# Performance work log

Measured on AMD Instinct MI355X. Metric: run time of the kernel, lower is better.

The kernel has to match this reference:

```python
import jax, jax.numpy as jnp
import numpy as np

INPUT_DIM = 362
HIDDEN = 256
STYLE_NUM = 60
OUTFIT_NUM = 49710
BATCH = 16384


def setup_inputs() -> dict:
    key = jax.random.key(0)
    ks = jax.random.split(key, 12)
    f32 = jnp.float32
    return {
        "i_feature": jax.random.normal(ks[0], (BATCH, INPUT_DIM), f32),
        "j_feature": jax.random.normal(ks[1], (BATCH, INPUT_DIM), f32),
        "k_feature": jax.random.normal(ks[2], (BATCH, INPUT_DIM), f32),
        # top_emb / bottom_emb Linear params (stored transposed: x @ W + b)
        "W_top": jax.random.normal(ks[3], (INPUT_DIM, HIDDEN), f32) * 0.05,
        "b_top": jnp.zeros((HIDDEN,), f32),
        "W_bot": jax.random.normal(ks[4], (INPUT_DIM, HIDDEN), f32) * 0.05,
        "b_bot": jnp.zeros((HIDDEN,), f32),
        # NMF factors (forward relu_'s them in place; we relu on use)
        "P_nmf": jax.random.normal(ks[5], (2 * INPUT_DIM, STYLE_NUM), f32),
        "N_nmf": jax.random.normal(ks[6], (2 * INPUT_DIM, STYLE_NUM), f32),
        "H1_nmf": jax.random.normal(ks[7], (STYLE_NUM, OUTFIT_NUM), f32),
        "H2_nmf": jax.random.normal(ks[8], (STYLE_NUM, OUTFIT_NUM), f32),
        "matirx_pos": jax.random.uniform(ks[9], (2 * INPUT_DIM, OUTFIT_NUM), f32),
        "matirx_neg": jax.random.uniform(ks[10], (2 * INPUT_DIM, OUTFIT_NUM), f32),
    }


def _emb(x, W, b):
    # nn.Sequential(Linear, Sigmoid)
    return jax.nn.sigmoid(x @ W + b)


def _style_score(i_f, j_f, styles, W_top, b_top, W_bot, b_bot):
    # Vectorized version of the per-sample loop:
    # squared-distance argmin codebook lookup + gather + rowwise dot.
    outfit = jnp.concatenate([i_f, j_f], axis=1)  # [B, 2D]
    # mean over feature dim of (x - s)^2; constant 1/(2D) scale does not change argmin
    d2 = (jnp.sum(outfit * outfit, axis=1, keepdims=True)
          - 2.0 * (outfit @ styles)
          + jnp.sum(styles * styles, axis=0, keepdims=True))  # [B, S]
    idx = jnp.argmin(d2, axis=1)                               # [B]
    sel = styles.T[idx]                                        # [B, 2D] gather
    top, bot = sel[:, :INPUT_DIM], sel[:, INPUT_DIM:]
    # diag(matmul) == rowwise dot
    return jnp.sum(_emb(top, W_top, b_top) * _emb(bot, W_bot, b_bot), axis=1)  # [B]


def reference(i_feature, j_feature, k_feature, W_top, b_top, W_bot, b_bot,
              P_nmf, N_nmf, H1_nmf, H2_nmf, matirx_pos, matirx_neg):
    Ti = _emb(i_feature, W_top, b_top)   # [B, H]
    Bj = _emb(j_feature, W_bot, b_bot)   # [B, H]
    Bk = _emb(k_feature, W_bot, b_bot)   # [B, H]
    # torch.diag(matmul(Ti, Bj.T)) == rowwise dot (avoids [B,B] intermediate)
    ij_score = jnp.sum(Ti * Bj, axis=1)  # [B]
    ik_score = jnp.sum(Ti * Bk, axis=1)  # [B]

    # forward does relu_ on .data before use
    P = jnp.maximum(P_nmf, 0.0)
    N = jnp.maximum(N_nmf, 0.0)
    H1 = jnp.maximum(H1_nmf, 0.0)
    H2 = jnp.maximum(H2_nmf, 0.0)

    style_ij = _style_score(i_feature, j_feature, P, W_top, b_top, W_bot, b_bot)
    style_ik = _style_score(i_feature, k_feature, N, W_top, b_top, W_bot, b_bot)

    # -mean(log(sigmoid(d))) computed stably
    loss1 = -jnp.mean(jax.nn.log_sigmoid(ij_score - ik_score))
    loss2 = -jnp.mean(jax.nn.log_sigmoid(style_ij - style_ik))
    loss3 = jnp.mean(jnp.square(matirx_pos - P @ H1)
                     + jnp.square(matirx_neg - N @ H2))
    loss = loss1 + loss2 + 0.1 * loss3

    ij_ik = jnp.stack([ij_score, ik_score], axis=1)  # [B, 2]
    auc = jnp.mean((jnp.argmax(ij_ik, axis=1) == 0).astype(jnp.float32))
    return (loss, loss1, loss2, loss3, auc)
```

## Files before the change

kernel.cpp:

```cpp
#include <hip/hip_runtime.h>
#include <math.h>

#define BATCH 16384
#define IND   362
#define KP    384
#define HID   256
#define STY   60
#define NOUT  49710
#define OUTP  51200
#define D2    724
#define D2P   768

#define NB_HR   3200
#define NB_CW   768
#define NB_CPN  384
#define NB_CF   9216
#define NB_CONV (NB_HR + NB_CW + NB_CPN + NB_CF)

#define NB_SS   120

#define N_DT    46
#define N_OC    25
#define OCHUNK  2048
#define NSTEP_CH 32
#define NB_M    (2 * N_DT * N_OC)

#define NB_EMB  1024
#define NB_SA   512
#define NB_HH   16
#define NB_PPB  2
#define NB_HEAD (NB_HH + NB_PPB)

typedef __bf16 bf16x8 __attribute__((ext_vector_type(8)));
typedef float  floatx4 __attribute__((ext_vector_type(4)));
typedef float  floatx2 __attribute__((ext_vector_type(2)));

__device__ inline floatx4 mfma16(bf16x8 a, bf16x8 b, floatx4 c) {
  return __builtin_amdgcn_mfma_f32_16x16x32_bf16(a, b, c, 0, 0, 0);
}

__device__ inline unsigned short f32_to_bf16(float x) {
  unsigned int u = __float_as_uint(x);
  unsigned int r = (u + 0x7FFFu + ((u >> 16) & 1u)) >> 16;
  return (unsigned short)r;
}

__device__ inline float sigm_fast(float x) { return 1.0f / (1.0f + __expf(-x)); }
__device__ inline float softplusf(float z) { return fmaxf(z, 0.0f) + log1pf(expf(-fabsf(z))); }

__global__ __launch_bounds__(256) void k_conv(
    const float* __restrict__ fi, const float* __restrict__ fj, const float* __restrict__ fk,
    const float* __restrict__ Wt, const float* __restrict__ Wb,
    const float* __restrict__ Pn, const float* __restrict__ Nn,
    const float* __restrict__ H1, const float* __restrict__ H2,
    unsigned short* __restrict__ fbf, unsigned short* __restrict__ wbfT,
    unsigned short* __restrict__ pnbfT, unsigned short* __restrict__ hrows) {
  int b = blockIdx.x;
  int t = threadIdx.x;

  if (b < NB_HR) {
    int e = (b * 256 + t) * 8;
    int row = e / OUTP;
    int o = e - row * OUTP;
    int s = row & 63;
    int mm = row >> 6;
    const float* H = mm ? H2 : H1;
    unsigned short* dst = hrows + (size_t)row * OUTP + o;
    unsigned int wv[4];
    if (s < STY && o + 8 <= NOUT) {
      const float* src = H + (size_t)s * NOUT + o;
      #pragma unroll
      for (int ee = 0; ee < 4; ee++) {
        floatx2 v = *(const floatx2*)(src + 2 * ee);
        wv[ee] = (unsigned)f32_to_bf16(fmaxf(v[0], 0.0f)) |
                 ((unsigned)f32_to_bf16(fmaxf(v[1], 0.0f)) << 16);
      }
    } else {
      #pragma unroll
      for (int ee = 0; ee < 4; ee++) {
        float lo = (s < STY && o + 2 * ee     < NOUT) ? fmaxf(H[(size_t)s * NOUT + o + 2 * ee],     0.0f) : 0.0f;
        float hi = (s < STY && o + 2 * ee + 1 < NOUT) ? fmaxf(H[(size_t)s * NOUT + o + 2 * ee + 1], 0.0f) : 0.0f;
        wv[ee] = (unsigned)f32_to_bf16(lo) | ((unsigned)f32_to_bf16(hi) << 16);
      }
    }
    uint4 v; v.x = wv[0]; v.y = wv[1]; v.z = wv[2]; v.w = wv[3];
    *(uint4*)dst = v;
    return;
  }
  b -= NB_HR;

  if (b < NB_CW) {
    int idx = b * 256 + t;
    int k = idx % KP;
    int rem = idx / KP;
    int h = rem % HID;
    int mm = rem / HID;
    const float* W = mm ? Wb : Wt;
    wbfT[idx] = f32_to_bf16(k < IND ? W[(size_t)k * HID + h] : 0.0f);
    return;
  }
  b -= NB_CW;

  if (b < NB_CPN) {
    int u = b * 256 + t;
    int s = u & 63;
    int v = u >> 6;
    int m = (v >= D2P) ? 1 : 0;
    int d = v - m * D2P;
    const float* M = m ? Nn : Pn;
    float x = (d < D2 && s < STY) ? fmaxf(M[(size_t)d * STY + s], 0.0f) : 0.0f;
    unsigned short bb = f32_to_bf16(x);
    int k = (d < IND) ? d : (d < D2 ? d + 22 : (d < 746 ? d - IND : d));
    pnbfT[((size_t)m * 64 + s) * D2P + k] = bb;
    return;
  }
  b -= NB_CPN;

  {
    long u = (long)b * 256 + t;
    int g = (int)(u % 48);
    long rf = u / 48;
    int row = (int)(rf % BATCH);
    int f = (int)(rf / BATCH);
    const float* src = (f == 0) ? fi : (f == 1 ? fj : fk);
    int d0 = g * 8;
    const float* sp = src + (size_t)row * IND + d0;
    unsigned int wv[4];
    #pragma unroll
    for (int e = 0; e < 4; e++) {
      int dd = d0 + 2 * e;
      float lo = (dd < IND)     ? sp[2 * e]     : 0.0f;
      float hi = (dd + 1 < IND) ? sp[2 * e + 1] : 0.0f;
      wv[e] = (unsigned)f32_to_bf16(lo) | ((unsigned)f32_to_bf16(hi) << 16);
    }
    uint4 v; v.x = wv[0]; v.y = wv[1]; v.z = wv[2]; v.w = wv[3];
    *(uint4*)(fbf + ((size_t)f * BATCH + row) * KP + d0) = v;
  }
}

__global__ __launch_bounds__(256) void k_style(
    const float* __restrict__ Wt, const float* __restrict__ btop,
    const float* __restrict__ Wb, const float* __restrict__ bbot,
    const float* __restrict__ Pn, const float* __restrict__ Nn,
    float* __restrict__ ss, float* __restrict__ cn) {
  __shared__ float sel[D2];
  __shared__ float shr[4];
  int b = blockIdx.x;
  int t = threadIdx.x;
  int s  = b % STY;
  int mt = b / STY;
  const float* M = mt ? Nn : Pn;
  float cnp = 0.0f;
  for (int d = t; d < D2; d += 256) {
    float v = fmaxf(M[(size_t)d * STY + s], 0.0f);
    sel[d] = v;
    cnp += v * v;
  }
  __syncthreads();
  float at = btop[t], ab = bbot[t];
  for (int d = 0; d < IND; d++) at = fmaf(sel[d],       Wt[(size_t)d * HID + t], at);
  for (int d = 0; d < IND; d++) ab = fmaf(sel[IND + d], Wb[(size_t)d * HID + t], ab);
  float prod = (1.0f / (1.0f + expf(-at))) * (1.0f / (1.0f + expf(-ab)));
  for (int off = 32; off > 0; off >>= 1) prod += __shfl_xor(prod, off);
  if ((t & 63) == 0) shr[t >> 6] = prod;
  __syncthreads();
  if (t == 0) ss[mt * 64 + s] = shr[0] + shr[1] + shr[2] + shr[3];
  __syncthreads();
  for (int off = 32; off > 0; off >>= 1) cnp += __shfl_xor(cnp, off);
  if ((t & 63) == 0) shr[t >> 6] = cnp;
  __syncthreads();
  if (t == 0) cn[mt * 64 + s] = shr[0] + shr[1] + shr[2] + shr[3];
}

__global__ __launch_bounds__(256, 4) void k_m(
    const unsigned short* __restrict__ hrows,
    const float* __restrict__ mp, const float* __restrict__ mneg,
    const float* __restrict__ Pn, const float* __restrict__ Nn,
    float* __restrict__ partial) {
  __shared__ float shp[4];
  int w = threadIdx.x >> 6, lane = threadIdx.x & 63;
  int m = lane & 15, q = lane >> 4;
  int b = blockIdx.x;
  int dt  = b % N_DT;
  int r   = b / N_DT;
  int oc  = r % N_OC;
  int mat = r / N_OC;
  int d0 = dt * 16, o0 = oc * OCHUNK;
  bool full = (o0 + OCHUNK <= NOUT);
  int d = d0 + m;
  bool rowok = (d < D2);
  const float* Mrow = (mat ? mneg : mp) + (size_t)d * NOUT;
  const unsigned short* Hb = hrows + ((size_t)mat * 64 + m) * OUTP;

  floatx4 acc[4];
  #pragma unroll
  for (int st = 0; st < 4; st++) acc[st] = (floatx4){0.f, 0.f, 0.f, 0.f};
  float msq = 0.0f;

  floatx2 mc[8], mn_[8];
  #pragma unroll
  for (int e = 0; e < 8; e++) { mc[e] = (floatx2){0.f, 0.f}; mn_[e] = (floatx2){0.f, 0.f}; }

  auto LOADM = [&](int j, floatx2* dst) {
    if (rowok) {
      if (full) {
        #pragma unroll
        for (int c = 0; c < 2; c++) {
          const float* Mr = Mrow + o0 + j * 64 + c * 32 + q * 8;
          dst[c * 4 + 0] = __builtin_nontemporal_load((const floatx2*)(Mr));
          dst[c * 4 + 1] = __builtin_nontemporal_load((const floatx2*)(Mr + 2));
          dst[c * 4 + 2] = __builtin_nontemporal_load((const floatx2*)(Mr + 4));
          dst[c * 4 + 3] = __builtin_nontemporal_load((const floatx2*)(Mr + 6));
        }
      } else {
        #pragma unroll
        for (int c = 0; c < 2; c++)
          #pragma unroll
          for (int e = 0; e < 4; e++) {
            int o = o0 + j * 64 + c * 32 + q * 8 + 2 * e;
            floatx2 v = {0.f, 0.f};
            if (o     < NOUT) v[0] = Mrow[o];
            if (o + 1 < NOUT) v[1] = Mrow[o + 1];
            dst[c * 4 + e] = v;
          }
      }
    } else {
      #pragma unroll
      for (int e = 0; e < 8; e++) dst[e] = (floatx2){0.f, 0.f};
    }
  };

  LOADM(w, mc);
  for (int j = w; j < NSTEP_CH; j += 4) {
    if (j + 4 < NSTEP_CH) LOADM(j + 4, mn_);
    bf16x8 h[2][4];
    #pragma unroll
    for (int c = 0; c < 2; c++)
      #pragma unroll
      for (int st = 0; st < 4; st++)
        h[c][st] = *(const bf16x8*)(Hb + (size_t)(st * 16) * OUTP + o0 + j * 64 + c * 32 + q * 8);
    #pragma unroll
    for (int c = 0; c < 2; c++) {
      union { unsigned int u32[4]; bf16x8 v; } cv;
      #pragma unroll
      for (int e = 0; e < 4; e++) {
        floatx2 tv = mc[c * 4 + e];
        msq = fmaf(tv[0], tv[0], msq);
        msq = fmaf(tv[1], tv[1], msq);
        cv.u32[e] = (unsigned)f32_to_bf16(tv[0]) | ((unsigned)f32_to_bf16(tv[1]) << 16);
      }
      #pragma unroll
      for (int st = 0; st < 4; st++) acc[st] = mfma16(cv.v, h[c][st], acc[st]);
    }
    #pragma unroll
    for (int e = 0; e < 8; e++) mc[e] = mn_[e];
  }

  const float* PM = mat ? Nn : Pn;
  float t2 = 0.0f;
  #pragma unroll
  for (int st = 0; st < 4; st++) {
    int s = st * 16 + m;
    if (s < STY) {
      #pragma unroll
      for (int rg = 0; rg < 4; rg++) {
        int dd = d0 + q * 4 + rg;
        if (dd < D2) {
          float pv = fmaxf(PM[(size_t)dd * STY + s], 0.0f);
          t2 = fmaf(pv, acc[st][rg], t2);
        }
      }
    }
  }
  float local = msq - 2.0f * t2;
  for (int off = 32; off > 0; off >>= 1) local += __shfl_xor(local, off);
  if (lane == 0) shp[w] = local;
  __syncthreads();
  if (threadIdx.x == 0) partial[blockIdx.x] = shp[0] + shp[1] + shp[2] + shp[3];
}

__global__ __launch_bounds__(256, 4) void k_emb(
    const unsigned short* __restrict__ fbf, const unsigned short* __restrict__ wbfT,
    const float* __restrict__ btop, const float* __restrict__ bbot,
    float* __restrict__ sIJ, float* __restrict__ sIK) {
  int w = threadIdx.x >> 6, lane = threadIdx.x & 63;
  int m = lane & 15, q = lane >> 4;
  int b = blockIdx.x;
  int r0 = (b & 255) * 64 + w * 16;
  int hb = (b >> 8) * 64;
  const unsigned short* fi = fbf + (size_t)(r0 + m) * KP + q * 8;
  const unsigned short* fj = fi + (size_t)BATCH * KP;
  const unsigned short* fk = fj + (size_t)BATCH * KP;
  floatx4 accI[4], accJ[4], accK[4];
  #pragma unroll
  for (int nt = 0; nt < 4; nt++) {
    accI[nt] = (floatx4){0.f, 0.f, 0.f, 0.f};
    accJ[nt] = (floatx4){0.f, 0.f, 0.f, 0.f};
    accK[nt] = (floatx4){0.f, 0.f, 0.f, 0.f};
  }
  for (int kc = 0; kc < 12; kc++) {
    bf16x8 ai = *(const bf16x8*)(fi + kc * 32);
    bf16x8 aj = *(const bf16x8*)(fj + kc * 32);
    bf16x8 ak = *(const bf16x8*)(fk + kc * 32);
    #pragma unroll
    for (int nt = 0; nt < 4; nt++) {
      int n = hb + nt * 16 + m;
      const unsigned short* wp = wbfT + (size_t)n * KP + kc * 32 + q * 8;
      bf16x8 bt8 = *(const bf16x8*)(wp);
      bf16x8 bb8 = *(const bf16x8*)(wp + (size_t)HID * KP);
      accI[nt] = mfma16(ai, bt8, accI[nt]);
      accJ[nt] = mfma16(aj, bb8, accJ[nt]);
      accK[nt] = mfma16(ak, bb8, accK[nt]);
    }
  }
  float sij[4] = {0.f, 0.f, 0.f, 0.f}, sik[4] = {0.f, 0.f, 0.f, 0.f};
  #pragma unroll
  for (int nt = 0; nt < 4; nt++) {
    int n = hb + nt * 16 + m;
    float vbt = btop[n], vbb = bbot[n];
    #pragma unroll
    for (int reg = 0; reg < 4; reg++) {
      float ti = sigm_fast(accI[nt][reg] + vbt);
      float tj = sigm_fast(accJ[nt][reg] + vbb);
      float tk = sigm_fast(accK[nt][reg] + vbb);
      sij[reg] += ti * tj;
      sik[reg] += ti * tk;
    }
  }
  #pragma unroll
  for (int reg = 0; reg < 4; reg++) {
    for (int off = 1; off < 16; off <<= 1) {
      sij[reg] += __shfl_xor(sij[reg], off);
      sik[reg] += __shfl_xor(sik[reg], off);
    }
  }
  if (m == 0) {
    #pragma unroll
    for (int reg = 0; reg < 4; reg++) {
      int row = r0 + q * 4 + reg;
      atomicAdd(&sIJ[row], sij[reg]);
      atomicAdd(&sIK[row], sik[reg]);
    }
  }
}

__global__ __launch_bounds__(256, 4) void k_sa(
    const unsigned short* __restrict__ fbf, const unsigned short* __restrict__ pnbfT,
    const float* __restrict__ cn, const float* __restrict__ ss,
    float* __restrict__ stIJ, float* __restrict__ stIK) {
  int w = threadIdx.x >> 6, lane = threadIdx.x & 63;
  int m = lane & 15, q = lane >> 4;
  int b = blockIdx.x;
  int mat = w & 1;
  int r0 = b * 32 + (w >> 1) * 16;
  const unsigned short* fA = fbf + (size_t)(r0 + m) * KP + q * 8;
  const unsigned short* fB = fA + (size_t)(1 + mat) * BATCH * KP;
  const unsigned short* Bp = pnbfT + (size_t)mat * 64 * D2P + q * 8;
  floatx4 acc[4];
  #pragma unroll
  for (int nt = 0; nt < 4; nt++) acc[nt] = (floatx4){0.f, 0.f, 0.f, 0.f};
  for (int kc = 0; kc < 24; kc++) {
    bf16x8 a = (kc < 12) ? *(const bf16x8*)(fA + kc * 32)
                         : *(const bf16x8*)(fB + (kc - 12) * 32);
    #pragma unroll
    for (int nt = 0; nt < 4; nt++) {
      bf16x8 bb = *(const bf16x8*)(Bp + (size_t)(nt * 16 + m) * D2P + kc * 32);
      acc[nt] = mfma16(a, bb, acc[nt]);
    }
  }
  const float* cnm = cn + mat * 64;
  float bv[4]; int bi[4];
  #pragma unroll
  for (int reg = 0; reg < 4; reg++) { bv[reg] = __builtin_inff(); bi[reg] = 1 << 30; }
  #pragma unroll
  for (int nt = 0; nt < 4; nt++) {
    int s = nt * 16 + m;
    float c = cnm[s & 63];
    #pragma unroll
    for (int reg = 0; reg < 4; reg++) {
      float d2 = (s < STY) ? (c - 2.0f * acc[nt][reg]) : __builtin_inff();
      if (d2 < bv[reg] || (d2 == bv[reg] && s < bi[reg])) { bv[reg] = d2; bi[reg] = s; }
    }
  }
  for (int off = 1; off < 16; off <<= 1) {
    #pragma unroll
    for (int reg = 0; reg < 4; reg++) {
      float ov = __shfl_xor(bv[reg], off);
      int   oi = __shfl_xor(bi[reg], off);
      if (ov < bv[reg] || (ov == bv[reg] && oi < bi[reg])) { bv[reg] = ov; bi[reg] = oi; }
    }
  }
  if (m == 0) {
    float* dst = mat ? stIK : stIJ;
    const float* ssm = ss + mat * 64;
    #pragma unroll
    for (int reg = 0; reg < 4; reg++) dst[r0 + q * 4 + reg] = ssm[bi[reg]];
  }
}

__global__ __launch_bounds__(256) void k_head(
    const unsigned short* __restrict__ pnbfT, const unsigned short* __restrict__ hrows,
    float* __restrict__ HHb, float* __restrict__ PPb) {
  __shared__ float red[4096];
  int w = threadIdx.x >> 6, lane = threadIdx.x & 63;
  int m = lane & 15, q = lane >> 4;
  int b = blockIdx.x;
  bool isPP = (b >= NB_HH);
  int mat, chunk, nsteps, stride;
  const unsigned short* Rb;
  if (!isPP) { mat = b >> 3; chunk = b & 7; Rb = hrows + (size_t)mat * 64 * OUTP; stride = OUTP; nsteps = 200; }
  else       { mat = b - NB_HH; chunk = 0; Rb = pnbfT + (size_t)mat * 64 * D2P;  stride = D2P;  nsteps = 24;  }
  const unsigned short* Rm = Rb + (size_t)m * stride;

  floatx4 acc[4][4];
  #pragma unroll
  for (int a2 = 0; a2 < 4; a2++)
    #pragma unroll
    for (int b2 = 0; b2 < 4; b2++) acc[a2][b2] = (floatx4){0.f, 0.f, 0.f, 0.f};

  bf16x8 hc[4], hn[4];
  auto LD = [&](int j, bf16x8* h) {
    int k = (chunk * nsteps + j) * 32 + q * 8;
    #pragma unroll
    for (int st = 0; st < 4; st++)
      h[st] = *(const bf16x8*)(Rm + (size_t)(st * 16) * stride + k);
  };
  int j = w;
  LD(j, hc);
  for (; j < nsteps; j += 4) {
    if (j + 4 < nsteps) LD(j + 4, hn);
    #pragma unroll
    for (int a2 = 0; a2 < 4; a2++)
      #pragma unroll
      for (int b2 = 0; b2 < 4; b2++)
        acc[a2][b2] = mfma16(hc[a2], hc[b2], acc[a2][b2]);
    #pragma unroll
    for (int st = 0; st < 4; st++) hc[st] = hn[st];
  }
  for (int idx = threadIdx.x; idx < 4096; idx += 256) red[idx] = 0.f;
  __syncthreads();
  #pragma unroll
  for (int a2 = 0; a2 < 4; a2++)
    #pragma unroll
    for (int b2 = 0; b2 < 4; b2++)
      #pragma unroll
      for (int r = 0; r < 4; r++)
        atomicAdd(&red[(a2 * 16 + q * 4 + r) * 64 + b2 * 16 + m], acc[a2][b2][r]);
  __syncthreads();
  float* dst = (isPP ? PPb : HHb) + (size_t)mat * 4096;
  for (int idx = threadIdx.x; idx < 4096; idx += 256) atomicAdd(&dst[idx], red[idx]);
}

__global__ __launch_bounds__(256) void k_final(
    const float* __restrict__ sIJ, const float* __restrict__ sIK,
    const float* __restrict__ stIJ, const float* __restrict__ stIK,
    const float* __restrict__ l3partial,
    const float* __restrict__ HHb, const float* __restrict__ PPb,
    float* __restrict__ out) {
  int t = threadIdx.x;
  float l1 = 0.f, l2 = 0.f, ac = 0.f;
  for (int r = t; r < BATCH; r += 256) {
    float dij = sIJ[r] - sIK[r];
    l1 += softplusf(-dij);
    if (dij >= 0.0f) ac += 1.0f;
    float dst = stIJ[r] - stIK[r];
    l2 += softplusf(-dst);
  }
  double l3 = 0.0;
  for (int p = t; p < NB_M; p += 256) l3 += (double)l3partial[p];
  for (int idx = t; idx < 8192; idx += 256) l3 += (double)HHb[idx] * (double)PPb[idx];
  __shared__ float sh1[4], sh2[4], sh3[4];
  __shared__ double sh4[4];
  for (int off = 32; off > 0; off >>= 1) {
    l1 += __shfl_xor(l1, off);
    l2 += __shfl_xor(l2, off);
    ac += __shfl_xor(ac, off);
    l3 += __shfl_xor(l3, off);
  }
  if ((t & 63) == 0) { sh1[t >> 6] = l1; sh2[t >> 6] = l2; sh3[t >> 6] = ac; sh4[t >> 6] = l3; }
  __syncthreads();
  if (t == 0) {
    double L1 = 0, L2 = 0, AC = 0, L3 = 0;
    for (int i = 0; i < 4; i++) { L1 += sh1[i]; L2 += sh2[i]; AC += sh3[i]; L3 += sh4[i]; }
    L1 /= BATCH; L2 /= BATCH; AC /= BATCH;
    L3 /= ((double)D2 * (double)NOUT);
    out[0] = (float)(L1 + L2 + 0.1 * L3);
    out[1] = (float)L1;
    out[2] = (float)L2;
    out[3] = (float)L3;
    out[4] = (float)AC;
  }
}

extern "C" void kernel_launch(void* const* d_in, const int* in_sizes, int n_in,
                              void* d_out, int out_size, void* d_ws, size_t ws_size,
                              hipStream_t stream) {
  (void)in_sizes; (void)n_in; (void)out_size; (void)ws_size;
  const float* i_f  = (const float*)d_in[0];
  const float* j_f  = (const float*)d_in[1];
  const float* k_f  = (const float*)d_in[2];
  const float* W_t  = (const float*)d_in[3];
  const float* b_t  = (const float*)d_in[4];
  const float* W_b  = (const float*)d_in[5];
  const float* b_b  = (const float*)d_in[6];
  const float* P_n  = (const float*)d_in[7];
  const float* N_n  = (const float*)d_in[8];
  const float* H1   = (const float*)d_in[9];
  const float* H2   = (const float*)d_in[10];
  const float* Mp   = (const float*)d_in[11];
  const float* Mn   = (const float*)d_in[12];
  float* out = (float*)d_out;
  char* ws = (char*)d_ws;

  const size_t OFF_FBF   = 0;
  const size_t OFF_WBFT  = OFF_FBF   + (size_t)3 * BATCH * KP * 2;
  const size_t OFF_PNBFT = OFF_WBFT  + (size_t)2 * HID * KP * 2;
  const size_t OFF_HROWS = OFF_PNBFT + (size_t)2 * 64 * D2P * 2;
  const size_t OFF_SIJ   = OFF_HROWS + (size_t)2 * 64 * OUTP * 2;
  const size_t OFF_SIK   = OFF_SIJ   + (size_t)BATCH * 4;
  const size_t OFF_HH    = OFF_SIK   + (size_t)BATCH * 4;
  const size_t OFF_PP    = OFF_HH    + (size_t)2 * 4096 * 4;
  const size_t OFF_STIJ  = OFF_PP    + (size_t)2 * 4096 * 4;
  const size_t OFF_STIK  = OFF_STIJ  + (size_t)BATCH * 4;
  const size_t OFF_SS    = OFF_STIK  + (size_t)BATCH * 4;
  const size_t OFF_CN    = OFF_SS    + 512;
  const size_t OFF_L3P   = OFF_CN    + 512;

  unsigned short* fbf   = (unsigned short*)(ws + OFF_FBF);
  unsigned short* wbfT  = (unsigned short*)(ws + OFF_WBFT);
  unsigned short* pnbfT = (unsigned short*)(ws + OFF_PNBFT);
  unsigned short* hrows = (unsigned short*)(ws + OFF_HROWS);
  float*  sIJ  = (float*)(ws + OFF_SIJ);
  float*  sIK  = (float*)(ws + OFF_SIK);
  float*  HHb  = (float*)(ws + OFF_HH);
  float*  PPb  = (float*)(ws + OFF_PP);
  float*  stIJ = (float*)(ws + OFF_STIJ);
  float*  stIK = (float*)(ws + OFF_STIK);
  float*  ss   = (float*)(ws + OFF_SS);
  float*  cn   = (float*)(ws + OFF_CN);
  float*  l3p  = (float*)(ws + OFF_L3P);

  hipMemsetAsync(ws + OFF_SIJ, 0, (size_t)BATCH * 4 * 2 + (size_t)4 * 4096 * 4, stream);

  k_conv<<<NB_CONV, 256, 0, stream>>>(i_f, j_f, k_f, W_t, W_b, P_n, N_n, H1, H2,
                                      fbf, wbfT, pnbfT, hrows);
  k_style<<<NB_SS, 256, 0, stream>>>(W_t, b_t, W_b, b_b, P_n, N_n, ss, cn);
  k_m<<<NB_M, 256, 0, stream>>>(hrows, Mp, Mn, P_n, N_n, l3p);
  k_emb<<<NB_EMB, 256, 0, stream>>>(fbf, wbfT, b_t, b_b, sIJ, sIK);
  k_sa<<<NB_SA, 256, 0, stream>>>(fbf, pnbfT, cn, ss, stIJ, stIK);
  k_head<<<NB_HEAD, 256, 0, stream>>>(pnbfT, hrows, HHb, PPb);
  k_final<<<1, 256, 0, stream>>>(sIJ, sIK, stIJ, stIK, l3p, HHb, PPb, out);
}
```

Measured before the change: 746.7 us.

## Restructure loss3 kernel to stage H chunk in LDS and sweep rows

The k_m kernel is reorganized so each block loads a 64x256 bf16 slice of H into swizzled shared memory once, then sweeps half of the 724 rows of the M matrix through it. Previously every block reloaded H from global for each 16-row tile. Relu'd P/N factors are now precomputed as a padded float layout in k_conv, so the epilogue reads them as vector loads instead of strided scalar loads. The H row padding is also reduced from 51200 to 49920 columns, which shrinks the conversion and head passes. The grid shrinks to 780 blocks and each thread holds 32 floatx2 of M in registers, which risks lower occupancy and less latency hiding on the dominant M stream.

```diff
diff --git a/kernel.cpp b/kernel.cpp
--- a/kernel.cpp
+++ b/kernel.cpp
@@ -7,11 +7,11 @@
 #define HID   256
 #define STY   60
 #define NOUT  49710
-#define OUTP  51200
+#define OUTP  49920
 #define D2    724
 #define D2P   768
 
-#define NB_HR   3200
+#define NB_HR   3120
 #define NB_CW   768
 #define NB_CPN  384
 #define NB_CF   9216
@@ -19,11 +19,11 @@
 
 #define NB_SS   120
 
-#define N_DT    46
-#define N_OC    25
-#define OCHUNK  2048
-#define NSTEP_CH 32
-#define NB_M    (2 * N_DT * N_OC)
+#define OCH     256
+#define N_OC    195
+#define DHALF   368
+#define NTILES  23
+#define NB_M    (2 * 2 * N_OC)
 
 #define NB_EMB  1024
 #define NB_SA   512
@@ -54,7 +54,8 @@
     const float* __restrict__ Pn, const float* __restrict__ Nn,
     const float* __restrict__ H1, const float* __restrict__ H2,
     unsigned short* __restrict__ fbf, unsigned short* __restrict__ wbfT,
-    unsigned short* __restrict__ pnbfT, unsigned short* __restrict__ hrows) {
+    unsigned short* __restrict__ pnbfT, unsigned short* __restrict__ hrows,
+    float* __restrict__ Pr) {
   int b = blockIdx.x;
   int t = threadIdx.x;
 
@@ -112,6 +113,7 @@
     unsigned short bb = f32_to_bf16(x);
     int k = (d < IND) ? d : (d < D2 ? d + 22 : (d < 746 ? d - IND : d));
     pnbfT[((size_t)m * 64 + s) * D2P + k] = bb;
+    Pr[((size_t)m * D2P + d) * 64 + s] = x;
     return;
   }
   b -= NB_CPN;
@@ -172,111 +174,118 @@
   if (t == 0) cn[mt * 64 + s] = shr[0] + shr[1] + shr[2] + shr[3];
 }
 
-__global__ __launch_bounds__(256, 4) void k_m(
-    const unsigned short* __restrict__ hrows,
+__global__ __launch_bounds__(256) void k_m(
+    const unsigned short* __restrict__ hrows, const float* __restrict__ Pr,
     const float* __restrict__ mp, const float* __restrict__ mneg,
-    const float* __restrict__ Pn, const float* __restrict__ Nn,
     float* __restrict__ partial) {
-  __shared__ float shp[4];
+  __shared__ unsigned short Hs[64 * OCH];
+  __shared__ float red[4];
   int w = threadIdx.x >> 6, lane = threadIdx.x & 63;
   int m = lane & 15, q = lane >> 4;
+
   int b = blockIdx.x;
-  int dt  = b % N_DT;
-  int r   = b / N_DT;
-  int oc  = r % N_OC;
-  int mat = r / N_OC;
-  int d0 = dt * 16, o0 = oc * OCHUNK;
-  bool full = (o0 + OCHUNK <= NOUT);
-  int d = d0 + m;
-  bool rowok = (d < D2);
-  const float* Mrow = (mat ? mneg : mp) + (size_t)d * NOUT;
-  const unsigned short* Hb = hrows + ((size_t)mat * 64 + m) * OUTP;
-
-  floatx4 acc[4];
-  #pragma unroll
-  for (int st = 0; st < 4; st++) acc[st] = (floatx4){0.f, 0.f, 0.f, 0.f};
-  float msq = 0.0f;
-
-  floatx2 mc[8], mn_[8];
-  #pragma unroll
-  for (int e = 0; e < 8; e++) { mc[e] = (floatx2){0.f, 0.f}; mn_[e] = (floatx2){0.f, 0.f}; }
-
-  auto LOADM = [&](int j, floatx2* dst) {
-    if (rowok) {
-      if (full) {
-        #pragma unroll
-        for (int c = 0; c < 2; c++) {
-          const float* Mr = Mrow + o0 + j * 64 + c * 32 + q * 8;
-          dst[c * 4 + 0] = __builtin_nontemporal_load((const floatx2*)(Mr));
-          dst[c * 4 + 1] = __builtin_nontemporal_load((const floatx2*)(Mr + 2));
-          dst[c * 4 + 2] = __builtin_nontemporal_load((const floatx2*)(Mr + 4));
-          dst[c * 4 + 3] = __builtin_nontemporal_load((const floatx2*)(Mr + 6));
-        }
-      } else {
-        #pragma unroll
-        for (int c = 0; c < 2; c++)
-          #pragma unroll
-          for (int e = 0; e < 4; e++) {
-            int o = o0 + j * 64 + c * 32 + q * 8 + 2 * e;
-            floatx2 v = {0.f, 0.f};
-            if (o     < NOUT) v[0] = Mrow[o];
-            if (o + 1 < NOUT) v[1] = Mrow[o + 1];
-            dst[c * 4 + e] = v;
-          }
+  int oc  = b % N_OC;
+  int r   = b / N_OC;
+  int dh  = r & 1;
+  int mat = r >> 1;
+  int o0 = oc * OCH;
+  bool full = (o0 + OCH <= NOUT);
+  const float* Mbase = mat ? mneg : mp;
+  const float* Prb   = Pr + (size_t)mat * D2P * 64;
+
+  char* HsB = (char*)Hs;
+  #pragma unroll
+  for (int rr = 0; rr < 16; rr++) {
+    int R = w * 16 + rr;
+    uint2 hv = *(const uint2*)(hrows + ((size_t)mat * 64 + R) * OUTP + o0 + lane * 4);
+    *(uint2*)(HsB + R * 512 + ((lane * 8) ^ ((R & 7) << 4))) = hv;
+  }
+  __syncthreads();
+
+  int xm = (m & 7) << 4;
+  float msq = 0.0f, t2 = 0.0f;
+  floatx2 mreg[32];
+  floatx4 preg[4];
+
+  auto ISSUE_M = [&](int t) {
+    int d = dh * DHALF + t * 16 + m;
+    bool ok = (d < D2);
+    const float* Mr = Mbase + (size_t)d * NOUT + o0 + q * 8;
+    if (ok && full) {
+      #pragma unroll
+      for (int kc = 0; kc < 8; kc++) {
+        mreg[kc * 4 + 0] = *(const floatx2*)(Mr + kc * 32);
+        mreg[kc * 4 + 1] = *(const floatx2*)(Mr + kc * 32 + 2);
+        mreg[kc * 4 + 2] = *(const floatx2*)(Mr + kc * 32 + 4);
+        mreg[kc * 4 + 3] = *(const floatx2*)(Mr + kc * 32 + 6);
       }
     } else {
       #pragma unroll
-      for (int e = 0; e < 8; e++) dst[e] = (floatx2){0.f, 0.f};
+      for (int kc = 0; kc < 8; kc++) {
+        #pragma unroll
+        for (int e = 0; e < 4; e++) {
+          int o = o0 + kc * 32 + q * 8 + 2 * e;
+          floatx2 v = {0.f, 0.f};
+          if (ok) {
+            if (o     < NOUT) v[0] = Mbase[(size_t)d * NOUT + o];
+            if (o + 1 < NOUT) v[1] = Mbase[(size_t)d * NOUT + o + 1];
+          }
+          mreg[kc * 4 + e] = v;
+        }
+      }
     }
   };
-
-  LOADM(w, mc);
-  for (int j = w; j < NSTEP_CH; j += 4) {
-    if (j + 4 < NSTEP_CH) LOADM(j + 4, mn_);
-    bf16x8 h[2][4];
-    #pragma unroll
-    for (int c = 0; c < 2; c++)
-      #pragma unroll
-      for (int st = 0; st < 4; st++)
-        h[c][st] = *(const bf16x8*)(Hb + (size_t)(st * 16) * OUTP + o0 + j * 64 + c * 32 + q * 8);
-    #pragma unroll
-    for (int c = 0; c < 2; c++) {
-      union { unsigned int u32[4]; bf16x8 v; } cv;
+  auto ISSUE_P = [&](int t) {
+    int d = dh * DHALF + t * 16 + m;
+    const float* Pp = Prb + (size_t)d * 64 + q * 4;
+    #pragma unroll
+    for (int st = 0; st < 4; st++) preg[st] = *(const floatx4*)(Pp + st * 16);
+  };
+
+  int t0 = w;
+  if (t0 < NTILES) { ISSUE_M(t0); ISSUE_P(t0); }
+  for (int t = t0; t < NTILES; t += 4) {
+    bf16x8 bf[8];
+    #pragma unroll
+    for (int kc = 0; kc < 8; kc++) {
+      union { unsigned int u[4]; bf16x8 v; } cv;
       #pragma unroll
       for (int e = 0; e < 4; e++) {
-        floatx2 tv = mc[c * 4 + e];
+        floatx2 tv = mreg[kc * 4 + e];
         msq = fmaf(tv[0], tv[0], msq);
         msq = fmaf(tv[1], tv[1], msq);
-        cv.u32[e] = (unsigned)f32_to_bf16(tv[0]) | ((unsigned)f32_to_bf16(tv[1]) << 16);
+        cv.u[e] = (unsigned)f32_to_bf16(tv[0]) | ((unsigned)f32_to_bf16(tv[1]) << 16);
       }
-      #pragma unroll
-      for (int st = 0; st < 4; st++) acc[st] = mfma16(cv.v, h[c][st], acc[st]);
-    }
-    #pragma unroll
-    for (int e = 0; e < 8; e++) mc[e] = mn_[e];
-  }
-
-  const float* PM = mat ? Nn : Pn;
-  float t2 = 0.0f;
-  #pragma unroll
-  for (int st = 0; st < 4; st++) {
-    int s = st * 16 + m;
-    if (s < STY) {
-      #pragma unroll
-      for (int rg = 0; rg < 4; rg++) {
-        int dd = d0 + q * 4 + rg;
-        if (dd < D2) {
-          float pv = fmaxf(PM[(size_t)dd * STY + s], 0.0f);
-          t2 = fmaf(pv, acc[st][rg], t2);
-        }
+      bf[kc] = cv.v;
+    }
+    int tn = t + 4;
+    if (tn < NTILES) ISSUE_M(tn);
+
+    floatx4 acc[4];
+    #pragma unroll
+    for (int st = 0; st < 4; st++) acc[st] = (floatx4){0.f, 0.f, 0.f, 0.f};
+    #pragma unroll
+    for (int kc = 0; kc < 8; kc++) {
+      #pragma unroll
+      for (int st = 0; st < 4; st++) {
+        bf16x8 hf = *(const bf16x8*)(HsB + (st * 16 + m) * 512 + ((kc * 64 + q * 16) ^ xm));
+        acc[st] = mfma16(hf, bf[kc], acc[st]);
       }
     }
-  }
+
+    #pragma unroll
+    for (int st = 0; st < 4; st++)
+      #pragma unroll
+      for (int rg = 0; rg < 4; rg++)
+        t2 = fmaf(preg[st][rg], acc[st][rg], t2);
+    if (tn < NTILES) ISSUE_P(tn);
+  }
+
   float local = msq - 2.0f * t2;
   for (int off = 32; off > 0; off >>= 1) local += __shfl_xor(local, off);
-  if (lane == 0) shp[w] = local;
-  __syncthreads();
-  if (threadIdx.x == 0) partial[blockIdx.x] = shp[0] + shp[1] + shp[2] + shp[3];
+  if (lane == 0) red[w] = local;
+  __syncthreads();
+  if (threadIdx.x == 0) partial[blockIdx.x] = red[0] + red[1] + red[2] + red[3];
 }
 
 __global__ __launch_bounds__(256, 4) void k_emb(
@@ -408,7 +417,7 @@
   bool isPP = (b >= NB_HH);
   int mat, chunk, nsteps, stride;
   const unsigned short* Rb;
-  if (!isPP) { mat = b >> 3; chunk = b & 7; Rb = hrows + (size_t)mat * 64 * OUTP; stride = OUTP; nsteps = 200; }
+  if (!isPP) { mat = b >> 3; chunk = b & 7; Rb = hrows + (size_t)mat * 64 * OUTP; stride = OUTP; nsteps = 195; }
   else       { mat = b - NB_HH; chunk = 0; Rb = pnbfT + (size_t)mat * 64 * D2P;  stride = D2P;  nsteps = 24;  }
   const unsigned short* Rm = Rb + (size_t)m * stride;
 
@@ -419,11 +428,11 @@
     for (int b2 = 0; b2 < 4; b2++) acc[a2][b2] = (floatx4){0.f, 0.f, 0.f, 0.f};
 
   bf16x8 hc[4], hn[4];
-  auto LD = [&](int j, bf16x8* h) {
+  auto LD = [&](int j, bf16x8* hh) {
     int k = (chunk * nsteps + j) * 32 + q * 8;
     #pragma unroll
     for (int st = 0; st < 4; st++)
-      h[st] = *(const bf16x8*)(Rm + (size_t)(st * 16) * stride + k);
+      hh[st] = *(const bf16x8*)(Rm + (size_t)(st * 16) * stride + k);
   };
   int j = w;
   LD(j, hc);
@@ -515,7 +524,8 @@
   const size_t OFF_FBF   = 0;
   const size_t OFF_WBFT  = OFF_FBF   + (size_t)3 * BATCH * KP * 2;
   const size_t OFF_PNBFT = OFF_WBFT  + (size_t)2 * HID * KP * 2;
-  const size_t OFF_HROWS = OFF_PNBFT + (size_t)2 * 64 * D2P * 2;
+  const size_t OFF_PR    = OFF_PNBFT + (size_t)2 * 64 * D2P * 2;
+  const size_t OFF_HROWS = OFF_PR    + (size_t)2 * D2P * 64 * 4;
   const size_t OFF_SIJ   = OFF_HROWS + (size_t)2 * 64 * OUTP * 2;
   const size_t OFF_SIK   = OFF_SIJ   + (size_t)BATCH * 4;
   const size_t OFF_HH    = OFF_SIK   + (size_t)BATCH * 4;
@@ -529,6 +539,7 @@
   unsigned short* fbf   = (unsigned short*)(ws + OFF_FBF);
   unsigned short* wbfT  = (unsigned short*)(ws + OFF_WBFT);
   unsigned short* pnbfT = (unsigned short*)(ws + OFF_PNBFT);
+  float*          Pr    = (float*)(ws + OFF_PR);
   unsigned short* hrows = (unsigned short*)(ws + OFF_HROWS);
   float*  sIJ  = (float*)(ws + OFF_SIJ);
   float*  sIK  = (float*)(ws + OFF_SIK);
@@ -543,9 +554,9 @@
   hipMemsetAsync(ws + OFF_SIJ, 0, (size_t)BATCH * 4 * 2 + (size_t)4 * 4096 * 4, stream);
 
   k_conv<<<NB_CONV, 256, 0, stream>>>(i_f, j_f, k_f, W_t, W_b, P_n, N_n, H1, H2,
-                                      fbf, wbfT, pnbfT, hrows);
+                                      fbf, wbfT, pnbfT, hrows, Pr);
   k_style<<<NB_SS, 256, 0, stream>>>(W_t, b_t, W_b, b_b, P_n, N_n, ss, cn);
-  k_m<<<NB_M, 256, 0, stream>>>(hrows, Mp, Mn, P_n, N_n, l3p);
+  k_m<<<NB_M, 256, 0, stream>>>(hrows, Pr, Mp, Mn, l3p);
   k_emb<<<NB_EMB, 256, 0, stream>>>(fbf, wbfT, b_t, b_b, sIJ, sIK);
   k_sa<<<NB_SA, 256, 0, stream>>>(fbf, pnbfT, cn, ss, stIJ, stIK);
   k_head<<<NB_HEAD, 256, 0, stream>>>(pnbfT, hrows, HHb, PPb);
```

After: 698.6 us. -6.4%, faster.
